# Performance work log

Measured on AMD Instinct MI355X. Metric: run time of the kernel, lower is better.

## Reference

```python
import jax, jax.numpy as jnp
import numpy as np

B, N, M = 2, 4096, 4096
DQ = DKV = DOUT = 512
HEADS, DH = 8, 64
INNER = HEADS * DH
SCALE = DH ** -0.5


def _ln(x, g, b, eps=1e-5):
    mu = jnp.mean(x, axis=-1, keepdims=True)
    var = jnp.mean(jnp.square(x - mu), axis=-1, keepdims=True)
    return (x - mu) * jax.lax.rsqrt(var + eps) * g + b


def setup_inputs() -> dict:
    key = jax.random.key(0)
    ks = jax.random.split(key, 12)
    s = lambda fan: 1.0 / np.sqrt(fan)
    return {
        "q0": jax.random.normal(ks[0], (B, N, DQ), jnp.float32),
        "kv0": jax.random.normal(ks[1], (B, M, DKV), jnp.float32),
        "normq_g": jnp.ones((DQ,), jnp.float32),
        "normq_b": jnp.zeros((DQ,), jnp.float32),
        "normkv_g": jnp.ones((DKV,), jnp.float32),
        "normkv_b": jnp.zeros((DKV,), jnp.float32),
        "Wq": jax.random.normal(ks[2], (DQ, INNER), jnp.float32) * s(DQ),
        "Wk": jax.random.normal(ks[3], (DKV, INNER), jnp.float32) * s(DKV),
        "Wv": jax.random.normal(ks[4], (DKV, INNER), jnp.float32) * s(DKV),
        "Wr": jax.random.normal(ks[5], (INNER, DQ), jnp.float32) * s(INNER),
        "mlp_g": jnp.ones((DQ,), jnp.float32),
        "mlp_b": jnp.zeros((DQ,), jnp.float32),
        "W1": jax.random.normal(ks[6], (DQ, DOUT), jnp.float32) * s(DQ),
        "b1": jnp.zeros((DOUT,), jnp.float32),
        "W2": jax.random.normal(ks[7], (DOUT, DOUT), jnp.float32) * s(DOUT),
        "b2": jnp.zeros((DOUT,), jnp.float32),
    }


def reference(q0, kv0, normq_g, normq_b, normkv_g, normkv_b,
              Wq, Wk, Wv, Wr, mlp_g, mlp_b, W1, b1, W2, b2):
    # projections
    q = _ln(q0, normq_g, normq_b) @ Wq                    # [B,N,INNER]
    kv = _ln(kv0, normkv_g, normkv_b)                     # [B,M,DKV]
    k = kv @ Wk                                           # [B,M,INNER]
    v = kv @ Wv                                           # [B,M,INNER]
    # split heads: b n (h d) -> b h n d
    q = q.reshape(B, N, HEADS, DH).transpose(0, 2, 1, 3)
    k = k.reshape(B, M, HEADS, DH).transpose(0, 2, 1, 3)
    v = v.reshape(B, M, HEADS, DH).transpose(0, 2, 1, 3)
    dots = jnp.einsum('bhnd,bhmd->bhnm', q, k) * SCALE    # [B,H,N,M]
    attn = jax.nn.softmax(dots, axis=-1)
    out = jnp.einsum('bhnm,bhmd->bhnd', attn, v)          # [B,H,N,DH]
    out = out.transpose(0, 2, 1, 3).reshape(B, N, INNER)  # b h n d -> b n (h d)
    out = out @ Wr + q0                                   # [B,N,DQ]
    # MLP branch with residual
    h = _ln(out, mlp_g, mlp_b)
    h = jax.nn.relu(h @ W1 + b1) @ W2 + b2
    return out + h
```

## Files before the change

kernel.cpp:

```cpp
#include <hip/hip_runtime.h>

typedef unsigned short u16;
typedef unsigned int u32;
typedef __bf16 bf16x8 __attribute__((ext_vector_type(8)));
typedef float f32x4 __attribute__((ext_vector_type(4)));
typedef u16 u16x8 __attribute__((ext_vector_type(8)));

#define SC2 0.18033688011112042f

__device__ __forceinline__ u16 bf16rne(float f) {
  u32 u = __float_as_uint(f);
  u32 r = (u + 0x7FFFu + ((u >> 16) & 1u)) >> 16;
  return (u16)r;
}
__device__ __forceinline__ u32 packrne(float a, float b) {
  return (u32)bf16rne(a) | ((u32)bf16rne(b) << 16);
}
__device__ __forceinline__ float b2f(u16 v) {
  return __uint_as_float(((u32)v) << 16);
}

__device__ __forceinline__ void async16(const void* g, void* l) {
  __builtin_amdgcn_global_load_lds(
      (__attribute__((address_space(1))) void*)(g),
      (__attribute__((address_space(3))) void*)(l), 16, 0, 0);
}
template <int N>
__device__ __forceinline__ void vm_wait() {
  asm volatile("s_waitcnt vmcnt(%0)" ::"n"(N) : "memory");
}
__device__ __forceinline__ void lgkm_wait0() {
  asm volatile("s_waitcnt lgkmcnt(0)" ::: "memory");
}
__device__ __forceinline__ void bar() {
  asm volatile("s_barrier" ::: "memory");
}

__device__ __forceinline__ void ln_row(const float* xr, const float* gp,
                                       const float* bp, u16* orow, int lane) {
  const float* xl = xr + lane * 8;
  float4 a0 = *(const float4*)xl;
  float4 a1 = *(const float4*)(xl + 4);
  float v[8] = {a0.x, a0.y, a0.z, a0.w, a1.x, a1.y, a1.z, a1.w};
  float s = 0.f, s2 = 0.f;
#pragma unroll
  for (int j = 0; j < 8; ++j) { s += v[j]; s2 += v[j] * v[j]; }
#pragma unroll
  for (int off = 32; off; off >>= 1) {
    s += __shfl_xor(s, off);
    s2 += __shfl_xor(s2, off);
  }
  float mu = s * (1.0f / 512.0f);
  float rstd = rsqrtf(s2 * (1.0f / 512.0f) - mu * mu + 1e-5f);
  const float* gl = gp + lane * 8;
  const float* bl = bp + lane * 8;
  float4 g0 = *(const float4*)gl, g1 = *(const float4*)(gl + 4);
  float4 b0 = *(const float4*)bl, b1 = *(const float4*)(bl + 4);
  float gg[8] = {g0.x, g0.y, g0.z, g0.w, g1.x, g1.y, g1.z, g1.w};
  float bb[8] = {b0.x, b0.y, b0.z, b0.w, b1.x, b1.y, b1.z, b1.w};
  u16x8 ov;
#pragma unroll
  for (int j = 0; j < 8; ++j) ov[j] = bf16rne((v[j] - mu) * rstd * gg[j] + bb[j]);
  *(u16x8*)(orow + lane * 8) = ov;
}

__global__ __launch_bounds__(256) void prep_kernel(
    const float* __restrict__ w0, const float* __restrict__ w1,
    const float* __restrict__ w2, const float* __restrict__ w3,
    const float* __restrict__ w4, const float* __restrict__ w5,
    u16* __restrict__ wout,
    const float* __restrict__ x0, const float* __restrict__ g0,
    const float* __restrict__ b0, u16* __restrict__ o0,
    const float* __restrict__ x1, const float* __restrict__ g1,
    const float* __restrict__ b1, u16* __restrict__ o1) {
  __shared__ u16 T[64 * 72];
  int t = threadIdx.x;
  int bx = blockIdx.x;
  if (bx < 384) {
    int widx = bx >> 6, tile = bx & 63;
    int k0 = (tile & 7) * 64, n0 = (tile >> 3) * 64;
    const float* W = w0;
    if (widx == 1) W = w1; else if (widx == 2) W = w2; else if (widx == 3) W = w3;
    else if (widx == 4) W = w4; else if (widx == 5) W = w5;
#pragma unroll
    for (int p = 0; p < 4; ++p) {
      int kr = p * 16 + (t >> 4);
      int nc = (t & 15) * 4;
      float4 v = *(const float4*)(W + (size_t)(k0 + kr) * 512 + n0 + nc);
      T[(nc + 0) * 72 + kr] = bf16rne(v.x);
      T[(nc + 1) * 72 + kr] = bf16rne(v.y);
      T[(nc + 2) * 72 + kr] = bf16rne(v.z);
      T[(nc + 3) * 72 + kr] = bf16rne(v.w);
    }
    __syncthreads();
    u16* ob = wout + (size_t)widx * 262144;
#pragma unroll
    for (int p = 0; p < 2; ++p) {
      int idx = p * 256 + t;
      int nr = idx >> 3, ch = idx & 7;
      uint4 val = *(const uint4*)(T + nr * 72 + ch * 8);
      *(uint4*)(ob + (size_t)(n0 + nr) * 512 + k0 + ch * 8) = val;
    }
  } else {
    int w = t >> 6, lane = t & 63;
    size_t row = (size_t)(bx - 384) * 4 + w;
    if (row < 8192) {
      ln_row(x0 + row * 512, g0, b0, o0 + row * 512, lane);
    } else {
      size_t r2 = row - 8192;
      ln_row(x1 + r2 * 512, g1, b1, o1 + r2 * 512, lane);
    }
  }
}

__global__ __launch_bounds__(256) void ln_kernel(
    const float* __restrict__ x, const float* __restrict__ g,
    const float* __restrict__ b, u16* __restrict__ o) {
  int w = threadIdx.x >> 6, lane = threadIdx.x & 63;
  size_t row = (size_t)blockIdx.x * 4 + w;
  ln_row(x + row * 512, g, b, o + row * 512, lane);
}

#define GSTAGE(buf, k0)                                                          \
  {                                                                              \
    _Pragma("unroll") for (int i = 0; i < 2; ++i) {                              \
      int s = t + 256 * i;                                                       \
      int mts = s >> 6, L = s & 63;                                             \
      async16(A + (size_t)(row0 + mts * 16 + (L & 15)) * 512 + (k0) + (L >> 4) * 8, \
              (char*)As[buf] + s * 16);                                          \
    }                                                                            \
    {                                                                            \
      int s = t;                                                                 \
      int nts = s >> 6, L = s & 63;                                             \
      async16(Bt + (size_t)(col0 + nts * 16 + (L & 15)) * 512 + (k0) + (L >> 4) * 8, \
              (char*)Bs[buf] + s * 16);                                          \
    }                                                                            \
  }

#define GEMM_CORE                                                                \
  GSTAGE(0, 0);                                                                  \
  GSTAGE(1, 32);                                                                 \
  GSTAGE(2, 64);                                                                 \
  _Pragma("unroll") for (int kk = 0; kk < 16; ++kk) {                            \
    if (kk <= 13) vm_wait<6>();                                                  \
    else if (kk == 14) vm_wait<3>();                                             \
    else vm_wait<0>();                                                           \
    bar();                                                                       \
    if (kk < 13) GSTAGE((kk + 3) & 3, (kk + 3) * 32);                            \
    const u16* Ac = As[kk & 3];                                                  \
    const u16* Bc = Bs[kk & 3];                                                  \
    bf16x8 Af[2], Bf[4];                                                         \
    _Pragma("unroll") for (int mt = 0; mt < 2; ++mt)                             \
        Af[mt] = *(const bf16x8*)(Ac + ((w * 2 + mt) * 64 + lane) * 8);          \
    _Pragma("unroll") for (int nt = 0; nt < 4; ++nt)                             \
        Bf[nt] = *(const bf16x8*)(Bc + (nt * 64 + lane) * 8);                    \
    _Pragma("unroll") for (int mt = 0; mt < 2; ++mt)                             \
        _Pragma("unroll") for (int nt = 0; nt < 4; ++nt)                         \
            acc[mt][nt] = __builtin_amdgcn_mfma_f32_16x16x32_bf16(               \
                Af[mt], Bf[nt], acc[mt][nt], 0, 0, 0);                           \
  }

template <int MODE>
__global__ __launch_bounds__(256) void gemm512_kernel(
    const u16* __restrict__ A, const u16* __restrict__ Bt, void* __restrict__ Cv,
    const float* __restrict__ bias, const float* __restrict__ res) {
  __shared__ __align__(16) u16 As[4][4096];
  __shared__ __align__(16) u16 Bs[4][2048];
  const int t = threadIdx.x;
  const int lane = t & 63;
  const int w = t >> 6;
  const int row0 = blockIdx.y * 128;
  const int col0 = blockIdx.x * 64;
  f32x4 acc[2][4];
#pragma unroll
  for (int i = 0; i < 2; ++i)
#pragma unroll
    for (int j = 0; j < 4; ++j) acc[i][j] = (f32x4){0.f, 0.f, 0.f, 0.f};

  GEMM_CORE

  const int q = lane >> 4, cl = lane & 15;
#pragma unroll
  for (int mt = 0; mt < 2; ++mt) {
#pragma unroll
    for (int nt = 0; nt < 4; ++nt) {
      int col = col0 + nt * 16 + cl;
#pragma unroll
      for (int r = 0; r < 4; ++r) {
        int row = row0 + (w * 2 + mt) * 16 + q * 4 + r;
        float v = acc[mt][nt][r];
        if (MODE == 1) {
          size_t idx = (size_t)row * 512 + col;
          ((float*)Cv)[idx] = v + res[idx];
        } else if (MODE == 2) {
          v += bias[col];
          ((u16*)Cv)[(size_t)row * 512 + col] = bf16rne(fmaxf(v, 0.f));
        } else {
          size_t idx = (size_t)row * 512 + col;
          ((float*)Cv)[idx] = v + bias[col] + res[idx];
        }
      }
    }
  }
}

__global__ __launch_bounds__(256) void proj_kernel(
    const u16* __restrict__ Aq, const u16* __restrict__ BtQ, u16* __restrict__ Qp,
    const u16* __restrict__ Akv, const u16* __restrict__ BtKV,
    u16* __restrict__ Kp, u16* __restrict__ VTp) {
  __shared__ __align__(16) u16 As[4][4096];
  __shared__ __align__(16) u16 Bs[4][2048];
  const int t = threadIdx.x;
  const int lane = t & 63;
  const int w = t >> 6;
  const int bx = blockIdx.x;
  const bool isq = bx < 8;
  const u16* A = isq ? Aq : Akv;
  const u16* Bt = isq ? BtQ : BtKV;
  const int row0 = blockIdx.y * 128;
  const int col0 = (isq ? bx : bx - 8) * 64;
  f32x4 acc[2][4];
#pragma unroll
  for (int i = 0; i < 2; ++i)
#pragma unroll
    for (int j = 0; j < 4; ++j) acc[i][j] = (f32x4){0.f, 0.f, 0.f, 0.f};

  GEMM_CORE

  const int q = lane >> 4, cl = lane & 15;
#pragma unroll
  for (int mt = 0; mt < 2; ++mt) {
#pragma unroll
    for (int nt = 0; nt < 4; ++nt) {
      int col = col0 + nt * 16 + cl;
      if (!isq && col >= 512) {
        int d = col - 512;
        int bb = row0 >> 12;
        int mloc = (row0 & 4095) + (w * 2 + mt) * 16 + q * 4;
        uint2 pk;
        pk.x = packrne(acc[mt][nt][0], acc[mt][nt][1]);
        pk.y = packrne(acc[mt][nt][2], acc[mt][nt][3]);
        *(uint2*)(VTp + ((size_t)bb * 512 + d) * 4096 + mloc) = pk;
        continue;
      }
#pragma unroll
      for (int r = 0; r < 4; ++r) {
        int row = row0 + (w * 2 + mt) * 16 + q * 4 + r;
        float v = acc[mt][nt][r];
        if (isq) {
          Qp[(size_t)row * 512 + col] = bf16rne(v * SC2);
        } else {
          Kp[(size_t)row * 512 + col] = bf16rne(v);
        }
      }
    }
  }
}

__global__ __launch_bounds__(128, 2) void attn_kernel(
    const u16* __restrict__ Q, const u16* __restrict__ K,
    const u16* __restrict__ VT, u16* __restrict__ O0, u16* __restrict__ O1,
    float* __restrict__ lpart) {
  __shared__ __align__(16) u16 Ks[2][4096];
  __shared__ __align__(16) u16 Vs[2][4096];
  __shared__ __align__(16) u16 Ps[2][1024];
  const int t = threadIdx.x;
  const int lane = t & 63;
  const int w = t >> 6;
  const int g = lane >> 4, cl = lane & 15;
  const int qt = blockIdx.x, h = blockIdx.y;
  const int b = blockIdx.z >> 1, sp = blockIdx.z & 1;
  const u16* Qg = Q + ((size_t)(b * 4096 + qt * 128 + w * 64)) * 512 + h * 64;
  const u16* Kg = K + ((size_t)(b * 4096 + sp * 2048)) * 512 + h * 64;
  const u16* VTg = VT + ((size_t)(b * 512 + h * 64)) * 4096 + sp * 2048;
  u16* Ob = (sp ? O1 : O0) + (((size_t)(b * 8 + h) * 4096) + qt * 128 + w * 64) * 64;
  float* lb = lpart + ((size_t)((sp * 2 + b) * 8 + h)) * 4096 + qt * 128 + w * 64;
  char* Pw = (char*)Ps[w];

#pragma unroll
  for (int i = 0; i < 8; ++i) {
    async16(Qg + (size_t)((i >> 1) * 16 + cl) * 512 + (i & 1) * 32 + g * 8,
            (char*)Ks[w] + (i * 64 + lane) * 16);
  }
  vm_wait<0>();
  bf16x8 Qb[4][2];
#pragma unroll
  for (int nt = 0; nt < 4; ++nt)
#pragma unroll
    for (int ks = 0; ks < 2; ++ks)
      Qb[nt][ks] = *(const bf16x8*)((char*)Ks[w] + ((nt * 2 + ks) * 64 + lane) * 16);
  lgkm_wait0();
  bar();

#define STAGEKV(buf, m0)                                                          \
  {                                                                               \
    _Pragma("unroll") for (int i = 0; i < 4; ++i) {                               \
      int s = t + 128 * i; int c = s >> 6; int L = s & 63;                        \
      async16(Kg + (size_t)((m0) + (c >> 1) * 16 + (L & 15)) * 512 + (c & 1) * 32 + (L >> 4) * 8, \
              (char*)Ks[buf] + s * 16);                                           \
    }                                                                             \
    _Pragma("unroll") for (int i = 0; i < 4; ++i) {                               \
      int s = t + 128 * i; int c = s >> 6; int L = s & 63;                        \
      async16(VTg + (size_t)((c >> 1) * 16 + (L & 15)) * 4096 + (m0) + (c & 1) * 32 + (L >> 4) * 8, \
              (char*)Vs[buf] + s * 16);                                           \
    }                                                                             \
  }

  STAGEKV(0, 0);

  u16x8 ou;
#pragma unroll
  for (int j = 0; j < 8; ++j) ou[j] = 0x3F80;
  bf16x8 ones = __builtin_bit_cast(bf16x8, ou);

  f32x4 Oa[4][4], ls[4];
#pragma unroll
  for (int i = 0; i < 4; ++i) {
    ls[i] = (f32x4){0.f, 0.f, 0.f, 0.f};
#pragma unroll
    for (int j = 0; j < 4; ++j) Oa[i][j] = (f32x4){0.f, 0.f, 0.f, 0.f};
  }
  const int s7 = cl & 7;

  for (int it = 0; it < 32; ++it) {
    if (it < 31) {
      STAGEKV((it + 1) & 1, (it + 1) * 64);
      vm_wait<8>();
    } else {
      vm_wait<0>();
    }
    bar();
    const u16* Kc = Ks[it & 1];
    const u16* Vc = Vs[it & 1];
    bf16x8 Kf[4][2], Vf[4][2];
#pragma unroll
    for (int mt = 0; mt < 4; ++mt)
#pragma unroll
      for (int ks = 0; ks < 2; ++ks) {
        Kf[mt][ks] = *(const bf16x8*)((const char*)Kc + ((mt * 2 + ks) * 64 + lane) * 16);
        Vf[mt][ks] = *(const bf16x8*)((const char*)Vc + ((mt * 2 + ks) * 64 + lane) * 16);
      }

#pragma unroll
    for (int nt = 0; nt < 4; ++nt) {
      f32x4 St[4];
#pragma unroll
      for (int mt = 0; mt < 4; ++mt) St[mt] = (f32x4){0.f, 0.f, 0.f, 0.f};
#pragma unroll
      for (int ks = 0; ks < 2; ++ks)
#pragma unroll
        for (int mt = 0; mt < 4; ++mt)
          St[mt] = __builtin_amdgcn_mfma_f32_16x16x32_bf16(Kf[mt][ks], Qb[nt][ks], St[mt], 0, 0, 0);

#pragma unroll
      for (int mt = 0; mt < 4; ++mt) {
        float p0 = __builtin_amdgcn_exp2f(St[mt][0]);
        float p1 = __builtin_amdgcn_exp2f(St[mt][1]);
        float p2 = __builtin_amdgcn_exp2f(St[mt][2]);
        float p3 = __builtin_amdgcn_exp2f(St[mt][3]);
        uint2 pk;
        pk.x = __builtin_amdgcn_perm(__float_as_uint(p1), __float_as_uint(p0), 0x07060302u);
        pk.y = __builtin_amdgcn_perm(__float_as_uint(p3), __float_as_uint(p2), 0x07060302u);
        *(uint2*)(Pw + cl * 128 + (((mt * 2 + (g >> 1)) ^ s7) << 4) + ((g & 1) << 3)) = pk;
      }
      bf16x8 Pb[2];
#pragma unroll
      for (int ks = 0; ks < 2; ++ks)
        Pb[ks] = *(const bf16x8*)(Pw + cl * 128 + (((ks * 4 + g) ^ s7) << 4));
      ls[nt] = __builtin_amdgcn_mfma_f32_16x16x32_bf16(ones, Pb[0], ls[nt], 0, 0, 0);
      ls[nt] = __builtin_amdgcn_mfma_f32_16x16x32_bf16(ones, Pb[1], ls[nt], 0, 0, 0);
#pragma unroll
      for (int ks = 0; ks < 2; ++ks)
#pragma unroll
        for (int mtd = 0; mtd < 4; ++mtd)
          Oa[mtd][nt] = __builtin_amdgcn_mfma_f32_16x16x32_bf16(Vf[mtd][ks], Pb[ks], Oa[mtd][nt], 0, 0, 0);
    }
    bar();
  }

#pragma unroll
  for (int nt = 0; nt < 4; ++nt) {
    int q = nt * 16 + cl;
#pragma unroll
    for (int mtd = 0; mtd < 4; ++mtd) {
      uint2 pk;
      pk.x = packrne(Oa[mtd][nt][0], Oa[mtd][nt][1]);
      pk.y = packrne(Oa[mtd][nt][2], Oa[mtd][nt][3]);
      *(uint2*)(Ob + (size_t)q * 64 + mtd * 16 + g * 4) = pk;
    }
    if (g == 0) lb[q] = ls[nt][0];
  }
}

__global__ __launch_bounds__(256) void combine_kernel(
    const u16* __restrict__ O0, const u16* __restrict__ O1,
    const float* __restrict__ lp, u16* __restrict__ out) {
  int idx = blockIdx.x * 256 + threadIdx.x;
  int dc = idx & 7;
  int q = (idx >> 3) & 4095;
  int h = (idx >> 15) & 7;
  int b = idx >> 18;
  size_t po = (((size_t)(b * 8 + h) * 4096) + q) * 64 + dc * 8;
  u16x8 a = *(const u16x8*)(O0 + po);
  u16x8 c = *(const u16x8*)(O1 + po);
  float l0 = lp[((size_t)(b * 8 + h)) * 4096 + q];
  float l1 = lp[((size_t)(16 + b * 8 + h)) * 4096 + q];
  float inv = 1.0f / (l0 + l1);
  u16x8 o;
#pragma unroll
  for (int j = 0; j < 8; ++j) o[j] = bf16rne((b2f(a[j]) + b2f(c[j])) * inv);
  *(u16x8*)(out + ((size_t)(b * 4096 + q)) * 512 + h * 64 + dc * 8) = o;
}

extern "C" void kernel_launch(void* const* d_in, const int* in_sizes, int n_in,
                              void* d_out, int out_size, void* d_ws, size_t ws_size,
                              hipStream_t stream) {
  const float* q0 = (const float*)d_in[0];
  const float* kv0 = (const float*)d_in[1];
  const float* nq_g = (const float*)d_in[2];
  const float* nq_b = (const float*)d_in[3];
  const float* nkv_g = (const float*)d_in[4];
  const float* nkv_b = (const float*)d_in[5];
  const float* Wq = (const float*)d_in[6];
  const float* Wk = (const float*)d_in[7];
  const float* Wv = (const float*)d_in[8];
  const float* Wr = (const float*)d_in[9];
  const float* mlp_g = (const float*)d_in[10];
  const float* mlp_b = (const float*)d_in[11];
  const float* W1 = (const float*)d_in[12];
  const float* b1 = (const float*)d_in[13];
  const float* W2 = (const float*)d_in[14];
  const float* b2 = (const float*)d_in[15];
  float* out = (float*)d_out;

  char* ws = (char*)d_ws;
  float* ob = (float*)(ws + 0);
  u16* O1p = (u16*)(ws + 0);
  u16* Qp = (u16*)(ws + 16777216);
  u16* aout = (u16*)(ws + 16777216);
  u16* Kp = (u16*)(ws + 25165824);
  u16* h1 = (u16*)(ws + 25165824);
  u16* VTp = (u16*)(ws + 33554432);
  u16* kvn2 = (u16*)(ws + 33554432);
  u16* wb = (u16*)(ws + 41943040);
  float* lpart = (float*)(ws + 45088768);
  u16* qn = (u16*)(ws + 46137344);
  u16* O0p = (u16*)(ws + 46137344);
  u16* kvn = (u16*)(ws + 54525952);
  u16* wqT = wb;
  u16* wkT = wb + 262144;
  u16* wrT = wb + 786432;
  u16* w1T = wb + 1048576;
  u16* w2T = wb + 1310720;

  dim3 blk(256);
  prep_kernel<<<4480, blk, 0, stream>>>(Wq, Wk, Wv, Wr, W1, W2, wb,
                                        q0, nq_g, nq_b, qn, kv0, nkv_g, nkv_b, kvn);
  proj_kernel<<<dim3(24, 64), blk, 0, stream>>>(qn, wqT, Qp, kvn, wkT, Kp, VTp);
  attn_kernel<<<dim3(32, 8, 4), dim3(128), 0, stream>>>(Qp, Kp, VTp, O0p, O1p, lpart);
  combine_kernel<<<2048, blk, 0, stream>>>(O0p, O1p, lpart, aout);
  gemm512_kernel<1><<<dim3(8, 64), blk, 0, stream>>>(aout, wrT, ob, nullptr, q0);
  ln_kernel<<<2048, blk, 0, stream>>>(ob, mlp_g, mlp_b, kvn2);
  gemm512_kernel<2><<<dim3(8, 64), blk, 0, stream>>>(kvn2, w1T, h1, b1, nullptr);
  gemm512_kernel<3><<<dim3(8, 64), blk, 0, stream>>>(h1, w2T, out, b2, ob);
}
```

Measured before the change: 296.2 us.

## Store post-attention residual in bf16 and swap grid axes for block ordering

```diff
diff --git a/kernel.cpp b/kernel.cpp
--- a/kernel.cpp
+++ b/kernel.cpp
@@ -42,6 +42,34 @@
   float4 a0 = *(const float4*)xl;
   float4 a1 = *(const float4*)(xl + 4);
   float v[8] = {a0.x, a0.y, a0.z, a0.w, a1.x, a1.y, a1.z, a1.w};
+  float s = 0.f, s2 = 0.f;
+#pragma unroll
+  for (int j = 0; j < 8; ++j) { s += v[j]; s2 += v[j] * v[j]; }
+#pragma unroll
+  for (int off = 32; off; off >>= 1) {
+    s += __shfl_xor(s, off);
+    s2 += __shfl_xor(s2, off);
+  }
+  float mu = s * (1.0f / 512.0f);
+  float rstd = rsqrtf(s2 * (1.0f / 512.0f) - mu * mu + 1e-5f);
+  const float* gl = gp + lane * 8;
+  const float* bl = bp + lane * 8;
+  float4 g0 = *(const float4*)gl, g1 = *(const float4*)(gl + 4);
+  float4 b0 = *(const float4*)bl, b1 = *(const float4*)(bl + 4);
+  float gg[8] = {g0.x, g0.y, g0.z, g0.w, g1.x, g1.y, g1.z, g1.w};
+  float bb[8] = {b0.x, b0.y, b0.z, b0.w, b1.x, b1.y, b1.z, b1.w};
+  u16x8 ov;
+#pragma unroll
+  for (int j = 0; j < 8; ++j) ov[j] = bf16rne((v[j] - mu) * rstd * gg[j] + bb[j]);
+  *(u16x8*)(orow + lane * 8) = ov;
+}
+
+__device__ __forceinline__ void lnb_row(const u16* xr, const float* gp,
+                                        const float* bp, u16* orow, int lane) {
+  u16x8 xv = *(const u16x8*)(xr + lane * 8);
+  float v[8];
+#pragma unroll
+  for (int j = 0; j < 8; ++j) v[j] = b2f(xv[j]);
   float s = 0.f, s2 = 0.f;
 #pragma unroll
   for (int j = 0; j < 8; ++j) { s += v[j]; s2 += v[j] * v[j]; }
@@ -113,12 +141,12 @@
   }
 }
 
-__global__ __launch_bounds__(256) void ln_kernel(
-    const float* __restrict__ x, const float* __restrict__ g,
+__global__ __launch_bounds__(256) void lnb_kernel(
+    const u16* __restrict__ x, const float* __restrict__ g,
     const float* __restrict__ b, u16* __restrict__ o) {
   int w = threadIdx.x >> 6, lane = threadIdx.x & 63;
   size_t row = (size_t)blockIdx.x * 4 + w;
-  ln_row(x + row * 512, g, b, o + row * 512, lane);
+  lnb_row(x + row * 512, g, b, o + row * 512, lane);
 }
 
 #define GSTAGE(buf, k0)                                                          \
@@ -169,8 +197,8 @@
   const int t = threadIdx.x;
   const int lane = t & 63;
   const int w = t >> 6;
-  const int row0 = blockIdx.y * 128;
-  const int col0 = blockIdx.x * 64;
+  const int row0 = blockIdx.x * 128;
+  const int col0 = blockIdx.y * 64;
   f32x4 acc[2][4];
 #pragma unroll
   for (int i = 0; i < 2; ++i)
@@ -189,15 +217,14 @@
       for (int r = 0; r < 4; ++r) {
         int row = row0 + (w * 2 + mt) * 16 + q * 4 + r;
         float v = acc[mt][nt][r];
-        if (MODE == 1) {
-          size_t idx = (size_t)row * 512 + col;
-          ((float*)Cv)[idx] = v + res[idx];
-        } else if (MODE == 2) {
+        size_t idx = (size_t)row * 512 + col;
+        if (MODE == 2) {
           v += bias[col];
-          ((u16*)Cv)[(size_t)row * 512 + col] = bf16rne(fmaxf(v, 0.f));
-        } else {
-          size_t idx = (size_t)row * 512 + col;
-          ((float*)Cv)[idx] = v + bias[col] + res[idx];
+          ((u16*)Cv)[idx] = bf16rne(fmaxf(v, 0.f));
+        } else if (MODE == 3) {
+          ((float*)Cv)[idx] = v + bias[col] + b2f(((const u16*)res)[idx]);
+        } else if (MODE == 7) {
+          ((u16*)Cv)[idx] = bf16rne(v + res[idx]);
         }
       }
     }
@@ -213,12 +240,12 @@
   const int t = threadIdx.x;
   const int lane = t & 63;
   const int w = t >> 6;
-  const int bx = blockIdx.x;
-  const bool isq = bx < 8;
+  const int by = blockIdx.y;
+  const bool isq = by < 8;
   const u16* A = isq ? Aq : Akv;
   const u16* Bt = isq ? BtQ : BtKV;
-  const int row0 = blockIdx.y * 128;
-  const int col0 = (isq ? bx : bx - 8) * 64;
+  const int row0 = blockIdx.x * 128;
+  const int col0 = (isq ? by : by - 8) * 64;
   f32x4 acc[2][4];
 #pragma unroll
   for (int i = 0; i < 2; ++i)
@@ -268,7 +295,7 @@
   const int lane = t & 63;
   const int w = t >> 6;
   const int g = lane >> 4, cl = lane & 15;
-  const int qt = blockIdx.x, h = blockIdx.y;
+  const int h = blockIdx.x, qt = blockIdx.y;
   const int b = blockIdx.z >> 1, sp = blockIdx.z & 1;
   const u16* Qg = Q + ((size_t)(b * 4096 + qt * 128 + w * 64)) * 512 + h * 64;
   const u16* Kg = K + ((size_t)(b * 4096 + sp * 2048)) * 512 + h * 64;
@@ -434,7 +461,7 @@
   float* out = (float*)d_out;
 
   char* ws = (char*)d_ws;
-  float* ob = (float*)(ws + 0);
+  u16* obb = (u16*)(ws + 0);
   u16* O1p = (u16*)(ws + 0);
   u16* Qp = (u16*)(ws + 16777216);
   u16* aout = (u16*)(ws + 16777216);
@@ -456,11 +483,11 @@
   dim3 blk(256);
   prep_kernel<<<4480, blk, 0, stream>>>(Wq, Wk, Wv, Wr, W1, W2, wb,
                                         q0, nq_g, nq_b, qn, kv0, nkv_g, nkv_b, kvn);
-  proj_kernel<<<dim3(24, 64), blk, 0, stream>>>(qn, wqT, Qp, kvn, wkT, Kp, VTp);
-  attn_kernel<<<dim3(32, 8, 4), dim3(128), 0, stream>>>(Qp, Kp, VTp, O0p, O1p, lpart);
+  proj_kernel<<<dim3(64, 24), blk, 0, stream>>>(qn, wqT, Qp, kvn, wkT, Kp, VTp);
+  attn_kernel<<<dim3(8, 32, 4), dim3(128), 0, stream>>>(Qp, Kp, VTp, O0p, O1p, lpart);
   combine_kernel<<<2048, blk, 0, stream>>>(O0p, O1p, lpart, aout);
-  gemm512_kernel<1><<<dim3(8, 64), blk, 0, stream>>>(aout, wrT, ob, nullptr, q0);
-  ln_kernel<<<2048, blk, 0, stream>>>(ob, mlp_g, mlp_b, kvn2);
-  gemm512_kernel<2><<<dim3(8, 64), blk, 0, stream>>>(kvn2, w1T, h1, b1, nullptr);
-  gemm512_kernel<3><<<dim3(8, 64), blk, 0, stream>>>(h1, w2T, out, b2, ob);
-}
+  gemm512_kernel<7><<<dim3(64, 8), blk, 0, stream>>>(aout, wrT, obb, nullptr, q0);
+  lnb_kernel<<<2048, blk, 0, stream>>>(obb, mlp_g, mlp_b, kvn2);
+  gemm512_kernel<2><<<dim3(64, 8), blk, 0, stream>>>(kvn2, w1T, h1, b1, nullptr);
+  gemm512_kernel<3><<<dim3(64, 8), blk, 0, stream>>>(h1, w2T, out, b2, (const float*)obb);
+}
```

Measured after the change: 286.4 us. -3.3%, faster.
